# Performance work log

Hardware: AMD Instinct MI355X
Metric: run time of the kernel (lower is better)

Reference implementation:

```python
import jax, jax.numpy as jnp
import numpy as np

B, T, D, H = 2, 2048, 1024, 16
DH = D // H  # 64


def setup_inputs() -> dict:
    key = jax.random.key(0)
    ks = jax.random.split(key, 8)
    s = 0.02  # typical init scale for projection weights
    return {
        "query_states": jax.random.normal(ks[0], (B, T, D), jnp.float32),
        "key_states": jax.random.normal(ks[1], (B, T, D), jnp.float32),
        "attention_mask": jnp.zeros((B, 1, 1, T), jnp.float32),
        "Wq": jax.random.normal(ks[2], (D, D), jnp.float32) * s,
        "bq": jnp.zeros((D,), jnp.float32),
        "Wk": jax.random.normal(ks[3], (D, D), jnp.float32) * s,
        "bk": jnp.zeros((D,), jnp.float32),
        "Wv": jax.random.normal(ks[4], (D, D), jnp.float32) * s,
        "bv": jnp.zeros((D,), jnp.float32),
        "mask_future": 0,
    }


def _heads(x):
    # [B, T, D] -> [B, H, T, DH]
    b, t, _ = x.shape
    return x.reshape(b, t, H, DH).transpose(0, 2, 1, 3)


def reference(query_states, key_states, attention_mask, Wq, bq, Wk, bk, Wv, bv, mask_future):
    q = _heads(query_states @ Wq + bq)   # [B,H,T,DH]
    k = _heads(key_states @ Wk + bk)     # [B,H,T,DH]
    v = _heads(key_states @ Wv + bv)     # [B,H,T,DH]
    scale = 1.0 / jnp.sqrt(jnp.asarray(DH, jnp.float32))
    scores = jnp.einsum("bhqd,bhkd->bhqk", q, k) * scale + attention_mask
    if mask_future:  # static Python int flag
        t = scores.shape[-1]
        triu = jnp.triu(jnp.ones((t, t), bool))  # includes diagonal, as in torch.triu
        scores = jnp.where(triu, -jnp.inf, scores)
    probs = jax.nn.softmax(scores, axis=-1)
    # dropout p=0.0 -> identity
    ctx = jnp.einsum("bhqk,bhkd->bhqd", probs, v)  # [B,H,T,DH]
    b, _, t, _ = ctx.shape
    return ctx.transpose(0, 2, 1, 3).reshape(b, t, H * DH)
```

## Files before the change

kernel.cpp:

```cpp
#include <hip/hip_runtime.h>

#define DEV __device__ __forceinline__

typedef _Float16 f16;
typedef __attribute__((ext_vector_type(2))) _Float16 f16x2;
typedef __attribute__((ext_vector_type(4))) _Float16 f16x4;
typedef __attribute__((ext_vector_type(8))) _Float16 f16x8;
typedef __attribute__((ext_vector_type(4))) float f32x4;
typedef __attribute__((ext_vector_type(16))) float f32x16;
typedef __attribute__((ext_vector_type(4))) int i32x4;

constexpr int B = 2, T = 2048, D = 1024, H = 16, DH = 64;
constexpr int M = B * T;
constexpr float LOG2E = 1.4426950408889634f;

DEV void gload_lds16(const void* g, void* l) {
  __builtin_amdgcn_global_load_lds(
      (const __attribute__((address_space(1))) void*)g,
      (__attribute__((address_space(3))) void*)l, 16, 0, 0);
}

DEV unsigned pack_pk(float a, float b) {
  auto v = __builtin_amdgcn_cvt_pkrtz(a, b);
  return __builtin_bit_cast(unsigned, v);
}

DEV float max3f(float a, float b, float c) { return fmaxf(fmaxf(a, b), c); }

#if __has_builtin(__builtin_amdgcn_permlane32_swap)
#define HAVE_PLSWAP 1
DEV void swap32(unsigned& a, unsigned& b) {
  auto r = __builtin_amdgcn_permlane32_swap((int)a, (int)b, false, false);
  a = (unsigned)r[0];
  b = (unsigned)r[1];
}
DEV float redmax32(float x) {
  unsigned a = __builtin_bit_cast(unsigned, x), b = a;
  swap32(a, b);
  return fmaxf(__builtin_bit_cast(float, a), __builtin_bit_cast(float, b));
}
DEV float redsum32(float x) {
  unsigned a = __builtin_bit_cast(unsigned, x), b = a;
  swap32(a, b);
  return __builtin_bit_cast(float, a) + __builtin_bit_cast(float, b);
}
#else
#define HAVE_PLSWAP 0
DEV float redmax32(float x) { return fmaxf(x, __shfl_xor(x, 32, 64)); }
DEV float redsum32(float x) { return x + __shfl_xor(x, 32, 64); }
#endif

__global__ __launch_bounds__(256) void cast_f32_f16(
    const float* __restrict__ in, f16* __restrict__ out, int n) {
  int i = (blockIdx.x * 256 + threadIdx.x) * 8;
  if (i >= n) return;
  f32x4 a = *(const f32x4*)(in + i);
  f32x4 b = *(const f32x4*)(in + i + 4);
  f16x8 o;
  o[0] = (f16)a[0]; o[1] = (f16)a[1]; o[2] = (f16)a[2]; o[3] = (f16)a[3];
  o[4] = (f16)b[0]; o[5] = (f16)b[1]; o[6] = (f16)b[2]; o[7] = (f16)b[3];
  *(f16x8*)(out + i) = o;
}

__global__ __launch_bounds__(256) void transpose_cast(
    const float* __restrict__ Wq, const float* __restrict__ Wk,
    const float* __restrict__ Wv, f16* __restrict__ WT) {
  int mat = blockIdx.z;
  const float* W = (mat == 0) ? Wq : (mat == 1 ? Wk : Wv);
  f16* out = WT + (size_t)mat * D * D;
  __shared__ float tile[32][33];
  int nt = blockIdx.x * 32, kt = blockIdx.y * 32;
  int tx = threadIdx.x, ty = threadIdx.y;
  for (int j = 0; j < 4; ++j) {
    int r = ty + 8 * j;
    tile[r][tx] = W[(size_t)(kt + r) * D + nt + tx];
  }
  __syncthreads();
  for (int j = 0; j < 4; ++j) {
    int r = ty + 8 * j;
    out[(size_t)(nt + r) * D + kt + tx] = (f16)tile[tx][r];
  }
}

__global__ __launch_bounds__(256) void qkv_gemm(
    const f16* __restrict__ XQ, const f16* __restrict__ XK,
    const f16* __restrict__ WT, const float* __restrict__ bq,
    const float* __restrict__ bk, const float* __restrict__ bv,
    f16* __restrict__ QKV) {
  int mat = blockIdx.z;
  const f16* X = (mat == 0) ? XQ : XK;
  const f16* Wt = WT + (size_t)mat * D * D;
  const float* bias = (mat == 0) ? bq : (mat == 1 ? bk : bv);
  f16* out = QKV + (size_t)mat * M * D;
  float oscale = (mat == 0) ? 0.125f * LOG2E : 1.0f;
  int Lb = blockIdx.x + 8 * blockIdx.y;
  int n0 = (Lb & 7) * 128, m0 = (Lb >> 3) * 128;

  __shared__ f16 lA[128 * 64];
  __shared__ f16 lB[128 * 64];
  char* lAb = (char*)lA;
  char* lBb = (char*)lB;

  int tid = threadIdx.x;
  int w = tid >> 6, lane = tid & 63;
  int l15 = lane & 15, lhi = lane >> 4;
  int wr = w >> 1, wc = w & 1;
  int r8 = lane >> 3, slot = lane & 7;
  int sslot = slot ^ r8;

  f32x4 acc[4][4] = {};

  for (int kt = 0; kt < D / 64; ++kt) {
    __syncthreads();
    for (int i = 0; i < 4; ++i) {
      int chunk = w * 4 + i;
      int row = chunk * 8 + r8;
      const f16* srcA = X + (size_t)(m0 + row) * D + kt * 64 + sslot * 8;
      gload_lds16(srcA, lAb + chunk * 1024);
      const f16* srcB = Wt + (size_t)(n0 + row) * D + kt * 64 + sslot * 8;
      gload_lds16(srcB, lBb + chunk * 1024);
    }
    __syncthreads();
    for (int ks = 0; ks < 2; ++ks) {
      f16x8 aF[4], bF[4];
      for (int mt = 0; mt < 4; ++mt) {
        int row = wr * 64 + mt * 16 + l15;
        int byt = (row * 128 + ks * 64 + lhi * 16) ^ ((row & 7) << 4);
        aF[mt] = *(const f16x8*)(lAb + byt);
      }
      for (int nt = 0; nt < 4; ++nt) {
        int row = wc * 64 + nt * 16 + l15;
        int byt = (row * 128 + ks * 64 + lhi * 16) ^ ((row & 7) << 4);
        bF[nt] = *(const f16x8*)(lBb + byt);
      }
      for (int mt = 0; mt < 4; ++mt)
        for (int nt = 0; nt < 4; ++nt)
          acc[mt][nt] = __builtin_amdgcn_mfma_f32_16x16x32_f16(
              aF[mt], bF[nt], acc[mt][nt], 0, 0, 0);
    }
  }

  float bv4[4];
  for (int nt = 0; nt < 4; ++nt) bv4[nt] = bias[n0 + wc * 64 + nt * 16 + l15];
  if (mat < 2) {
    for (int mt = 0; mt < 4; ++mt)
      for (int nt = 0; nt < 4; ++nt) {
        int col = n0 + wc * 64 + nt * 16 + l15;
        int hh = col >> 6, dh = col & 63;
        for (int r = 0; r < 4; ++r) {
          int row = m0 + wr * 64 + mt * 16 + lhi * 4 + r;
          int bb = row >> 11, tt = row & (T - 1);
          out[((size_t)(bb * H + hh) * T + tt) * 64 + dh] =
              (f16)((acc[mt][nt][r] + bv4[nt]) * oscale);
        }
      }
  } else {
    for (int mt = 0; mt < 4; ++mt)
      for (int nt = 0; nt < 4; ++nt) {
        int col = n0 + wc * 64 + nt * 16 + l15;
        int hh = col >> 6, dh = col & 63;
        int row0 = m0 + wr * 64 + mt * 16 + lhi * 4;
        int bb = row0 >> 11, tt = row0 & (T - 1);
        f16x4 pk;
        for (int r = 0; r < 4; ++r) pk[r] = (f16)(acc[mt][nt][r] + bv4[nt]);
        *(f16x4*)(out + ((size_t)(bb * H + hh) * 64 + dh) * T + tt) = pk;
      }
  }
}

__global__ __launch_bounds__(256) void attn(
    const f16* __restrict__ QKV, const float* __restrict__ mask,
    const int* __restrict__ mfp, float* __restrict__ out) {
  int L = blockIdx.x + 16 * blockIdx.y + 256 * blockIdx.z;
  int e = L & 7, q = L >> 3;
  int bh = e * 4 + (q & 3);
  int q0 = (q >> 2) * 128;
  int b = bh >> 4, h = bh & 15;
  int mf = *mfp;
  constexpr int NT = T / 64;

  const f16* Qh = QKV + (size_t)bh * T * 64;
  const f16* Kh = QKV + (size_t)M * D + (size_t)bh * T * 64;
  const f16* VTh = QKV + (size_t)2 * M * D + (size_t)bh * 64 * T;

  __shared__ char smem[32768];

  int tid = threadIdx.x;
  int w = tid >> 6, lane = tid & 63;
  int l31 = lane & 31, hi = lane >> 5;
  int qrow = q0 + w * 32 + l31;

  const float* mb = mask + (size_t)b * T;
  bool lnz = false;
#pragma unroll
  for (int j = 0; j < 8; ++j) {
    f32x4 mv = *(const f32x4*)(mb + lane * 32 + j * 4);
    lnz |= (mv[0] != 0.f) | (mv[1] != 0.f) | (mv[2] != 0.f) | (mv[3] != 0.f);
  }
  int domask = __any(lnz) | mf;

  f16x8 qF[4];
  const f16* qp = Qh + (size_t)qrow * 64;
#pragma unroll
  for (int kc = 0; kc < 4; ++kc) qF[kc] = *(const f16x8*)(qp + kc * 16 + hi * 8);

  auto STAGE = [&](int kv0, int buf) {
    char* dK = smem + buf * 8192;
    char* dV = smem + 16384 + buf * 8192;
#pragma unroll
    for (int i = 0; i < 2; ++i) {
      int c = (w * 2 + i) * 64 + lane;
      int r = c >> 3;
      int slot = (c & 7) ^ (r & 7);
      gload_lds16(Kh + (size_t)(kv0 + r) * 64 + slot * 8, dK + (w * 2 + i) * 1024);
      gload_lds16(VTh + (size_t)r * T + kv0 + slot * 8, dV + (w * 2 + i) * 1024);
    }
  };

  float mprev = -1e30f, lsum = 0.f;
  f32x16 oAcc[2] = {};
  STAGE(0, 0);
  __syncthreads();

  for (int t = 0; t < NT; ++t) {
    if (t) __syncthreads();
    if (t + 1 < NT) STAGE((t + 1) * 64, (t + 1) & 1);
    int kv0 = t * 64;
    const char* bK = smem + (t & 1) * 8192;
    const char* bV = smem + 16384 + (t & 1) * 8192;

    f32x16 sA[2] = {};
    __builtin_amdgcn_s_setprio(1);
#pragma unroll
    for (int f = 0; f < 2; ++f)
#pragma unroll
      for (int kc = 0; kc < 4; ++kc) {
        int row = f * 32 + l31;
        f16x8 kF = *(const f16x8*)(bK + ((row * 128 + kc * 32 + hi * 16) ^ ((row & 7) << 4)));
        sA[f] = __builtin_amdgcn_mfma_f32_32x32x16_f16(kF, qF[kc], sA[f], 0, 0, 0);
      }
    __builtin_amdgcn_s_setprio(0);

    float mx;
    if (domask) {
      mx = -1e30f;
#pragma unroll
      for (int f = 0; f < 2; ++f)
#pragma unroll
        for (int r = 0; r < 16; ++r) {
          int kv = kv0 + f * 32 + (r & 3) + 8 * (r >> 2) + 4 * hi;
          float v = sA[f][r] + LOG2E * mb[kv];
          if (mf && kv >= qrow) v = -1e30f;
          sA[f][r] = v;
          mx = fmaxf(mx, v);
        }
    } else {
      float t0 = max3f(sA[0][0], sA[0][1], sA[0][2]);
      float t1 = max3f(sA[0][3], sA[0][4], sA[0][5]);
      float t2 = max3f(sA[0][6], sA[0][7], sA[0][8]);
      float t3 = max3f(sA[0][9], sA[0][10], sA[0][11]);
      float t4 = max3f(sA[0][12], sA[0][13], sA[0][14]);
      float t5 = max3f(sA[1][0], sA[1][1], sA[1][2]);
      float t6 = max3f(sA[1][3], sA[1][4], sA[1][5]);
      float t7 = max3f(sA[1][6], sA[1][7], sA[1][8]);
      float t8 = max3f(sA[1][9], sA[1][10], sA[1][11]);
      float t9 = max3f(sA[1][12], sA[1][13], sA[1][14]);
      float u0 = max3f(t0, t1, t2);
      float u1 = max3f(t3, t4, sA[0][15]);
      float u2 = max3f(t5, t6, t7);
      float u3 = max3f(t8, t9, sA[1][15]);
      mx = fmaxf(max3f(u0, u1, u2), u3);
    }
    mx = redmax32(mx);

    if (!__all(mx <= mprev + 8.f)) {
      float mn = fmaxf(mprev, mx);
      float asc = __builtin_amdgcn_exp2f(mprev - mn);
      lsum *= asc;
#pragma unroll
      for (int f = 0; f < 2; ++f)
#pragma unroll
        for (int r = 0; r < 16; ++r) oAcc[f][r] *= asc;
      mprev = mn;
    }

    float rs = 0.f;
#pragma unroll
    for (int f = 0; f < 2; ++f)
#pragma unroll
      for (int r = 0; r < 16; ++r) {
        float e2 = __builtin_amdgcn_exp2f(sA[f][r] - mprev);
        sA[f][r] = e2;
        rs += e2;
      }
    lsum += redsum32(rs);

    f16x8 pF[4];
#if HAVE_PLSWAP
#pragma unroll
    for (int f = 0; f < 2; ++f)
#pragma unroll
      for (int half = 0; half < 2; ++half) {
        unsigned p0 = pack_pk(sA[f][half * 8 + 0], sA[f][half * 8 + 1]);
        unsigned p1 = pack_pk(sA[f][half * 8 + 2], sA[f][half * 8 + 3]);
        unsigned p2 = pack_pk(sA[f][half * 8 + 4], sA[f][half * 8 + 5]);
        unsigned p3 = pack_pk(sA[f][half * 8 + 6], sA[f][half * 8 + 7]);
        swap32(p0, p2);
        swap32(p1, p3);
        i32x4 d;
        d[0] = (int)p0; d[1] = (int)p1; d[2] = (int)p2; d[3] = (int)p3;
        pF[f * 2 + half] = __builtin_bit_cast(f16x8, d);
      }
#else
#pragma unroll
    for (int f = 0; f < 2; ++f) {
      unsigned pk_[8], px_[8];
#pragma unroll
      for (int g = 0; g < 8; ++g) {
        pk_[g] = pack_pk(sA[f][2 * g], sA[f][2 * g + 1]);
        px_[g] = (unsigned)__shfl_xor((int)pk_[g], 32, 64);
      }
#pragma unroll
      for (int half = 0; half < 2; ++half) {
        int o = half * 4;
        i32x4 d;
        d[0] = (int)(hi ? px_[o + 2] : pk_[o + 0]);
        d[1] = (int)(hi ? px_[o + 3] : pk_[o + 1]);
        d[2] = (int)(hi ? pk_[o + 2] : px_[o + 0]);
        d[3] = (int)(hi ? pk_[o + 3] : px_[o + 1]);
        pF[f * 2 + half] = __builtin_bit_cast(f16x8, d);
      }
    }
#endif

    __builtin_amdgcn_s_setprio(1);
#pragma unroll
    for (int df = 0; df < 2; ++df)
#pragma unroll
      for (int kc = 0; kc < 4; ++kc) {
        int row = df * 32 + l31;
        f16x8 vF = *(const f16x8*)(bV + ((row * 128 + kc * 32 + hi * 16) ^ ((row & 7) << 4)));
        oAcc[df] = __builtin_amdgcn_mfma_f32_32x32x16_f16(vF, pF[kc], oAcc[df], 0, 0, 0);
      }
    __builtin_amdgcn_s_setprio(0);
  }

  __syncthreads();
  float linv = 1.0f / lsum;
  float* sOw = (float*)smem + w * 2048;
#pragma unroll
  for (int df = 0; df < 2; ++df)
#pragma unroll
    for (int r = 0; r < 16; ++r) {
      int d = df * 32 + 4 * hi + (r & 3) + 8 * (r >> 2);
      sOw[l31 * 64 + (d ^ l31)] = oAcc[df][r] * linv;
    }
  __syncthreads();
  float* op0 = out + (size_t)(b * T + q0 + w * 32) * D + h * 64;
#pragma unroll
  for (int r2 = 0; r2 < 32; ++r2) {
    float v = sOw[r2 * 64 + (lane ^ r2)];
    op0[(size_t)r2 * D + lane] = v;
  }
}

extern "C" void kernel_launch(void* const* d_in, const int* in_sizes, int n_in,
                              void* d_out, int out_size, void* d_ws, size_t ws_size,
                              hipStream_t stream) {
  const float* q_in = (const float*)d_in[0];
  const float* k_in = (const float*)d_in[1];
  const float* amask = (const float*)d_in[2];
  const float* Wq = (const float*)d_in[3];
  const float* bq = (const float*)d_in[4];
  const float* Wk = (const float*)d_in[5];
  const float* bk = (const float*)d_in[6];
  const float* Wv = (const float*)d_in[7];
  const float* bv = (const float*)d_in[8];
  const int* mf = (const int*)d_in[9];
  float* out = (float*)d_out;

  char* ws = (char*)d_ws;
  f16* XQ = (f16*)ws;
  f16* XK = (f16*)(ws + (((size_t)8) << 20));
  f16* WT = (f16*)(ws + (((size_t)16) << 20));
  f16* QKV = (f16*)(ws + (((size_t)24) << 20));

  cast_f32_f16<<<2048, 256, 0, stream>>>(q_in, XQ, M * D);
  cast_f32_f16<<<2048, 256, 0, stream>>>(k_in, XK, M * D);
  transpose_cast<<<dim3(32, 32, 3), dim3(32, 8), 0, stream>>>(Wq, Wk, Wv, WT);
  qkv_gemm<<<dim3(8, 32, 3), 256, 0, stream>>>(XQ, XK, WT, bq, bk, bv, QKV);
  attn<<<dim3(16, 16, 2), 256, 0, stream>>>(QKV, amask, mf, out);
}
```

Baseline: 214.9 us.

## Merge prep kernels and load attention K/V directly into registers per wave

The two casts and the weight transpose are merged into a single prep launch to cut launch overhead. The attention kernel is restructured from 4-wave blocks sharing double-buffered LDS K/V tiles into single-wave blocks that load K and V fragments straight from global memory into registers. This removes LDS staging and block barriers, but each wave now fetches its own K/V with no reuse across waves and no prefetch overlap, so global/L2 traffic rises. The GEMM loops also get explicit unroll pragmas.

```diff
diff --git a/kernel.cpp b/kernel.cpp
--- a/kernel.cpp
+++ b/kernel.cpp
@@ -50,27 +50,33 @@
 DEV float redsum32(float x) { return x + __shfl_xor(x, 32, 64); }
 #endif
 
-__global__ __launch_bounds__(256) void cast_f32_f16(
-    const float* __restrict__ in, f16* __restrict__ out, int n) {
-  int i = (blockIdx.x * 256 + threadIdx.x) * 8;
-  if (i >= n) return;
-  f32x4 a = *(const f32x4*)(in + i);
-  f32x4 b = *(const f32x4*)(in + i + 4);
-  f16x8 o;
-  o[0] = (f16)a[0]; o[1] = (f16)a[1]; o[2] = (f16)a[2]; o[3] = (f16)a[3];
-  o[4] = (f16)b[0]; o[5] = (f16)b[1]; o[6] = (f16)b[2]; o[7] = (f16)b[3];
-  *(f16x8*)(out + i) = o;
-}
-
-__global__ __launch_bounds__(256) void transpose_cast(
+__global__ __launch_bounds__(256) void prep(
+    const float* __restrict__ qin, const float* __restrict__ kin,
     const float* __restrict__ Wq, const float* __restrict__ Wk,
-    const float* __restrict__ Wv, f16* __restrict__ WT) {
-  int mat = blockIdx.z;
+    const float* __restrict__ Wv, f16* __restrict__ XQK,
+    f16* __restrict__ WT) {
+  int bi = blockIdx.x;
+  int tid = threadIdx.x;
+  if (bi < 4096) {
+    const float* in = (bi < 2048) ? qin : kin;
+    f16* out = XQK + ((bi < 2048) ? 0 : (size_t)M * D);
+    int i = ((bi & 2047) * 256 + tid) * 8;
+    f32x4 a = *(const f32x4*)(in + i);
+    f32x4 b = *(const f32x4*)(in + i + 4);
+    f16x8 o;
+    o[0] = (f16)a[0]; o[1] = (f16)a[1]; o[2] = (f16)a[2]; o[3] = (f16)a[3];
+    o[4] = (f16)b[0]; o[5] = (f16)b[1]; o[6] = (f16)b[2]; o[7] = (f16)b[3];
+    *(f16x8*)(out + i) = o;
+    return;
+  }
+  int t = bi - 4096;
+  int mat = t >> 10;
+  int rem = t & 1023;
+  int nt = (rem & 31) * 32, kt = (rem >> 5) * 32;
   const float* W = (mat == 0) ? Wq : (mat == 1 ? Wk : Wv);
   f16* out = WT + (size_t)mat * D * D;
   __shared__ float tile[32][33];
-  int nt = blockIdx.x * 32, kt = blockIdx.y * 32;
-  int tx = threadIdx.x, ty = threadIdx.y;
+  int tx = tid & 31, ty = tid >> 5;
   for (int j = 0; j < 4; ++j) {
     int r = ty + 8 * j;
     tile[r][tx] = W[(size_t)(kt + r) * D + nt + tx];
@@ -112,28 +118,34 @@
 
   for (int kt = 0; kt < D / 64; ++kt) {
     __syncthreads();
+#pragma unroll
     for (int i = 0; i < 4; ++i) {
       int chunk = w * 4 + i;
       int row = chunk * 8 + r8;
-      const f16* srcA = X + (size_t)(m0 + row) * D + kt * 64 + sslot * 8;
-      gload_lds16(srcA, lAb + chunk * 1024);
-      const f16* srcB = Wt + (size_t)(n0 + row) * D + kt * 64 + sslot * 8;
-      gload_lds16(srcB, lBb + chunk * 1024);
+      gload_lds16(X + (size_t)(m0 + row) * D + kt * 64 + sslot * 8,
+                  lAb + chunk * 1024);
+      gload_lds16(Wt + (size_t)(n0 + row) * D + kt * 64 + sslot * 8,
+                  lBb + chunk * 1024);
     }
     __syncthreads();
+#pragma unroll
     for (int ks = 0; ks < 2; ++ks) {
       f16x8 aF[4], bF[4];
+#pragma unroll
       for (int mt = 0; mt < 4; ++mt) {
         int row = wr * 64 + mt * 16 + l15;
         int byt = (row * 128 + ks * 64 + lhi * 16) ^ ((row & 7) << 4);
         aF[mt] = *(const f16x8*)(lAb + byt);
       }
+#pragma unroll
       for (int nt = 0; nt < 4; ++nt) {
         int row = wc * 64 + nt * 16 + l15;
         int byt = (row * 128 + ks * 64 + lhi * 16) ^ ((row & 7) << 4);
         bF[nt] = *(const f16x8*)(lBb + byt);
       }
+#pragma unroll
       for (int mt = 0; mt < 4; ++mt)
+#pragma unroll
         for (int nt = 0; nt < 4; ++nt)
           acc[mt][nt] = __builtin_amdgcn_mfma_f32_16x16x32_f16(
               aF[mt], bF[nt], acc[mt][nt], 0, 0, 0);
@@ -168,13 +180,13 @@
   }
 }
 
-__global__ __launch_bounds__(256) void attn(
+__global__ __launch_bounds__(64) void attn(
     const f16* __restrict__ QKV, const float* __restrict__ mask,
     const int* __restrict__ mfp, float* __restrict__ out) {
-  int L = blockIdx.x + 16 * blockIdx.y + 256 * blockIdx.z;
+  int L = blockIdx.x;
   int e = L & 7, q = L >> 3;
   int bh = e * 4 + (q & 3);
-  int q0 = (q >> 2) * 128;
+  int q0 = (q >> 2) * 32;
   int b = bh >> 4, h = bh & 15;
   int mf = *mfp;
   constexpr int NT = T / 64;
@@ -183,12 +195,11 @@
   const f16* Kh = QKV + (size_t)M * D + (size_t)bh * T * 64;
   const f16* VTh = QKV + (size_t)2 * M * D + (size_t)bh * 64 * T;
 
-  __shared__ char smem[32768];
-
-  int tid = threadIdx.x;
-  int w = tid >> 6, lane = tid & 63;
+  __shared__ float sOw[2048];
+
+  int lane = threadIdx.x;
   int l31 = lane & 31, hi = lane >> 5;
-  int qrow = q0 + w * 32 + l31;
+  int qrow = q0 + l31;
 
   const float* mb = mask + (size_t)b * T;
   bool lnz = false;
@@ -204,42 +215,35 @@
 #pragma unroll
   for (int kc = 0; kc < 4; ++kc) qF[kc] = *(const f16x8*)(qp + kc * 16 + hi * 8);
 
-  auto STAGE = [&](int kv0, int buf) {
-    char* dK = smem + buf * 8192;
-    char* dV = smem + 16384 + buf * 8192;
-#pragma unroll
-    for (int i = 0; i < 2; ++i) {
-      int c = (w * 2 + i) * 64 + lane;
-      int r = c >> 3;
-      int slot = (c & 7) ^ (r & 7);
-      gload_lds16(Kh + (size_t)(kv0 + r) * 64 + slot * 8, dK + (w * 2 + i) * 1024);
-      gload_lds16(VTh + (size_t)r * T + kv0 + slot * 8, dV + (w * 2 + i) * 1024);
-    }
-  };
-
   float mprev = -1e30f, lsum = 0.f;
   f32x16 oAcc[2] = {};
-  STAGE(0, 0);
-  __syncthreads();
 
   for (int t = 0; t < NT; ++t) {
-    if (t) __syncthreads();
-    if (t + 1 < NT) STAGE((t + 1) * 64, (t + 1) & 1);
     int kv0 = t * 64;
-    const char* bK = smem + (t & 1) * 8192;
-    const char* bV = smem + 16384 + (t & 1) * 8192;
+
+    f16x8 kF[8];
+#pragma unroll
+    for (int f = 0; f < 2; ++f)
+#pragma unroll
+      for (int kc = 0; kc < 4; ++kc)
+        kF[f * 4 + kc] = *(const f16x8*)(
+            Kh + (size_t)(kv0 + f * 32 + l31) * 64 + kc * 16 + hi * 8);
+
+    f16x8 vF[8];
+#pragma unroll
+    for (int df = 0; df < 2; ++df)
+#pragma unroll
+      for (int kc = 0; kc < 4; ++kc)
+        vF[df * 4 + kc] = *(const f16x8*)(
+            VTh + (size_t)(df * 32 + l31) * T + kv0 + kc * 16 + hi * 8);
 
     f32x16 sA[2] = {};
-    __builtin_amdgcn_s_setprio(1);
 #pragma unroll
     for (int f = 0; f < 2; ++f)
 #pragma unroll
-      for (int kc = 0; kc < 4; ++kc) {
-        int row = f * 32 + l31;
-        f16x8 kF = *(const f16x8*)(bK + ((row * 128 + kc * 32 + hi * 16) ^ ((row & 7) << 4)));
-        sA[f] = __builtin_amdgcn_mfma_f32_32x32x16_f16(kF, qF[kc], sA[f], 0, 0, 0);
-      }
-    __builtin_amdgcn_s_setprio(0);
+      for (int kc = 0; kc < 4; ++kc)
+        sA[f] = __builtin_amdgcn_mfma_f32_32x32x16_f16(kF[f * 4 + kc], qF[kc],
+                                                       sA[f], 0, 0, 0);
 
     float mx;
     if (domask) {
@@ -333,21 +337,15 @@
     }
 #endif
 
-    __builtin_amdgcn_s_setprio(1);
 #pragma unroll
     for (int df = 0; df < 2; ++df)
 #pragma unroll
-      for (int kc = 0; kc < 4; ++kc) {
-        int row = df * 32 + l31;
-        f16x8 vF = *(const f16x8*)(bV + ((row * 128 + kc * 32 + hi * 16) ^ ((row & 7) << 4)));
-        oAcc[df] = __builtin_amdgcn_mfma_f32_32x32x16_f16(vF, pF[kc], oAcc[df], 0, 0, 0);
-      }
-    __builtin_amdgcn_s_setprio(0);
-  }
-
-  __syncthreads();
+      for (int kc = 0; kc < 4; ++kc)
+        oAcc[df] = __builtin_amdgcn_mfma_f32_32x32x16_f16(vF[df * 4 + kc],
+                                                          pF[kc], oAcc[df], 0, 0, 0);
+  }
+
   float linv = 1.0f / lsum;
-  float* sOw = (float*)smem + w * 2048;
 #pragma unroll
   for (int df = 0; df < 2; ++df)
 #pragma unroll
@@ -356,7 +354,7 @@
       sOw[l31 * 64 + (d ^ l31)] = oAcc[df][r] * linv;
     }
   __syncthreads();
-  float* op0 = out + (size_t)(b * T + q0 + w * 32) * D + h * 64;
+  float* op0 = out + (size_t)(b * T + q0) * D + h * 64;
 #pragma unroll
   for (int r2 = 0; r2 < 32; ++r2) {
     float v = sOw[r2 * 64 + (lane ^ r2)];
@@ -380,14 +378,12 @@
   float* out = (float*)d_out;
 
   char* ws = (char*)d_ws;
-  f16* XQ = (f16*)ws;
-  f16* XK = (f16*)(ws + (((size_t)8) << 20));
+  f16* XQK = (f16*)ws;
   f16* WT = (f16*)(ws + (((size_t)16) << 20));
   f16* QKV = (f16*)(ws + (((size_t)24) << 20));
 
-  cast_f32_f16<<<2048, 256, 0, stream>>>(q_in, XQ, M * D);
-  cast_f32_f16<<<2048, 256, 0, stream>>>(k_in, XK, M * D);
-  transpose_cast<<<dim3(32, 32, 3), dim3(32, 8), 0, stream>>>(Wq, Wk, Wv, WT);
-  qkv_gemm<<<dim3(8, 32, 3), 256, 0, stream>>>(XQ, XK, WT, bq, bk, bv, QKV);
-  attn<<<dim3(16, 16, 2), 256, 0, stream>>>(QKV, amask, mf, out);
-}
+  prep<<<7168, 256, 0, stream>>>(q_in, k_in, Wq, Wk, Wv, XQK, WT);
+  qkv_gemm<<<dim3(8, 32, 3), 256, 0, stream>>>(XQK, XQK + (size_t)M * D, WT, bq,
+                                               bk, bv, QKV);
+  attn<<<2048, 64, 0, stream>>>(QKV, amask, mf, out);
+}
```

Result: slower. 264.7 us (+23.2%).
